# Optimization experiments

Hardware: AMD Instinct MI355X
Metric: run time of the kernel (lower is better)

## Reference

```python
import jax, jax.numpy as jnp
import numpy as np

ADAPT_RATE = 0.05


def setup_inputs() -> dict:
    key = jax.random.key(0)
    k1, k2, k3 = jax.random.split(key, 3)
    B, T, DIN, DOUT = 64, 256, 1024, 1024
    x = jax.random.normal(k1, (B, T, DIN), dtype=jnp.float32)
    W = jax.random.normal(k2, (DOUT, DIN), dtype=jnp.float32) / np.sqrt(DIN)
    b = jax.random.normal(k3, (DOUT,), dtype=jnp.float32) * 0.01
    threshold = jnp.ones((DOUT,), dtype=jnp.float32)
    return {"x": x, "W": W, "b": b, "threshold": threshold}


def reference(x, W, b, threshold):
    # Precompute the per-timestep linear once as a single big GEMM: [B,T,O]
    pre = jnp.einsum('bti,oi->bto', x, W) + b
    B, T, O = pre.shape

    def step(carry, pre_t):
        mem, thr = carry
        mem = mem + pre_t                       # membrane accumulate [B,O]
        s = (mem >= thr).astype(pre_t.dtype)    # hard threshold spike
        # adaptive threshold: in-place .data update in torch (no grad path)
        thr = thr + ADAPT_RATE * (s.mean(axis=0) - 0.5)
        mem = mem * (1.0 - s)                   # reset where spiked
        return (mem, thr), s

    mem0 = jnp.zeros((B, O), dtype=x.dtype)
    (_, _), spikes = jax.lax.scan(step, (mem0, threshold), jnp.swapaxes(pre, 0, 1))
    return jnp.swapaxes(spikes, 0, 1)  # [B,T,O]
```

## Files before the change

### kernel.cpp

```cpp
#include <hip/hip_runtime.h>

#define B_ 64
#define T_ 256
#define DIN_ 1024
#define DOUT_ 1024

typedef int v4i  __attribute__((ext_vector_type(4)));
typedef int v16i __attribute__((ext_vector_type(16)));

#define PRE_BYTES 134217728ULL
#define XS_BYTES  83886080ULL
#define WSL_BYTES 5242880ULL
#define SPM_BYTES 2097152ULL

__device__ __forceinline__ void async_copy16(const void* g, void* l) {
    __builtin_amdgcn_global_load_lds(
        (const __attribute__((address_space(1))) void*)g,
        (__attribute__((address_space(3))) void*)l, 16, 0, 0);
}

__global__ __launch_bounds__(256) void snn_split_x(
    const float* __restrict__ x, char* __restrict__ xs)
{
    const int W    = blockIdx.x * 4 + (threadIdx.x >> 6);
    const int lane = threadIdx.x & 63;
    const int mt = W & 1, kt = (W >> 1) & 31, t0 = W >> 6;
    const int m = lane & 31, kh = lane >> 5;
    const int b = mt * 32 + m;

    const float* src = x + ((size_t)b * T_ + t0) * DIN_ + kt * 32 + kh * 16;
    float f[16];
    *(float4*)(f)      = *(const float4*)(src);
    *(float4*)(f + 4)  = *(const float4*)(src + 4);
    *(float4*)(f + 8)  = *(const float4*)(src + 8);
    *(float4*)(f + 12) = *(const float4*)(src + 12);

    unsigned pk[5][4];
#pragma unroll
    for (int s = 0; s < 5; ++s)
        pk[s][0] = pk[s][1] = pk[s][2] = pk[s][3] = 0u;
#pragma unroll
    for (int j = 0; j < 16; ++j) {
        float v = f[j] * 0.125f;
#pragma unroll
        for (int s = 0; s < 5; ++s) {
            const float ml = (s == 0) ? 64.f : 128.f;
            const float sv = __builtin_rintf(v * ml);
            v = v * ml - sv;
            const int iv = (int)sv;
            pk[s][j >> 2] |= ((unsigned)iv & 0xffu) << ((j & 3) * 8);
        }
    }
#pragma unroll
    for (int s = 0; s < 5; ++s) {
        char* dst = xs + (size_t)(((s * 256 + t0) * 32 + kt) * 2 + mt) * 1024
                       + lane * 16;
        *(uint4*)dst = make_uint4(pk[s][0], pk[s][1], pk[s][2], pk[s][3]);
    }
}

__global__ __launch_bounds__(256) void snn_split_w(
    const float* __restrict__ Wt, char* __restrict__ wsl)
{
    const int W    = blockIdx.x * 4 + (threadIdx.x >> 6);
    const int lane = threadIdx.x & 63;
    const int kt = W & 31, ot = W >> 5;
    const int n = lane & 31, kh = lane >> 5;
    const int o = ot * 32 + n;

    const float* src = Wt + (size_t)o * DIN_ + kt * 32 + kh * 16;
    float f[16];
    *(float4*)(f)      = *(const float4*)(src);
    *(float4*)(f + 4)  = *(const float4*)(src + 4);
    *(float4*)(f + 8)  = *(const float4*)(src + 8);
    *(float4*)(f + 12) = *(const float4*)(src + 12);

    unsigned pk[5][4];
#pragma unroll
    for (int s = 0; s < 5; ++s)
        pk[s][0] = pk[s][1] = pk[s][2] = pk[s][3] = 0u;
#pragma unroll
    for (int j = 0; j < 16; ++j) {
        float v = f[j] * 4.0f;
#pragma unroll
        for (int s = 0; s < 5; ++s) {
            const float ml = (s == 0) ? 64.f : 128.f;
            const float sv = __builtin_rintf(v * ml);
            v = v * ml - sv;
            const int iv = (int)sv;
            pk[s][j >> 2] |= ((unsigned)iv & 0xffu) << ((j & 3) * 8);
        }
    }
#pragma unroll
    for (int s = 0; s < 5; ++s) {
        char* dst = wsl + (size_t)((s * 32 + ot) * 32 + kt) * 1024 + lane * 16;
        *(uint4*)dst = make_uint4(pk[s][0], pk[s][1], pk[s][2], pk[s][3]);
    }
}

__global__ __launch_bounds__(256, 3) void snn_gemm_i8(
    const char* __restrict__ xs, const char* __restrict__ wsl,
    const float* __restrict__ bias, double* __restrict__ pre)
{
    __shared__ __align__(16) char lds[2][20 * 1024];
    const int t0 = blockIdx.x >> 4;
    const int oB = blockIdx.x & 15;
    const int tid = threadIdx.x;
    const int lane = tid & 63;
    const int ws = __builtin_amdgcn_readfirstlane(tid >> 6);
    const int wmS = ws >> 1, woS = ws & 1;

    v16i zero;
#pragma unroll
    for (int r = 0; r < 16; ++r) zero[r] = 0;
    v16i acc[5];
#pragma unroll
    for (int g = 0; g < 5; ++g) acc[g] = zero;

    const char* gbase;
    size_t sStride;
    int ktStride, slot0;
    if (ws < 2) {
        gbase   = xs + ((size_t)t0 * 32 * 2 + ws) * 1024;
        sStride = 16777216;
        ktStride = 2048;
        slot0 = ws * 5;
    } else {
        gbase   = wsl + (size_t)(oB * 2 + (ws - 2)) * 32 * 1024;
        sStride = 1048576;
        ktStride = 1024;
        slot0 = 10 + (ws - 2) * 5;
    }
    const int lo = lane * 16;

#pragma unroll
    for (int s = 0; s < 5; ++s)
        async_copy16(gbase + (size_t)s * sStride + lo,
                     &lds[0][(slot0 + s) * 1024]);

    for (int kt = 0; kt < 32; ++kt) {
        __syncthreads();
        if (kt + 1 < 32) {
            const char* gn = gbase + (size_t)(kt + 1) * ktStride;
#pragma unroll
            for (int s = 0; s < 5; ++s)
                async_copy16(gn + (size_t)s * sStride + lo,
                             &lds[(kt + 1) & 1][(slot0 + s) * 1024]);
        }
        const char* abase = &lds[kt & 1][(wmS * 5) * 1024] + lo;
        const char* bbase = &lds[kt & 1][(10 + woS * 5) * 1024] + lo;
        v4i a[5], b[5];
#pragma unroll
        for (int s = 0; s < 5; ++s) {
            a[s] = *(const v4i*)(abase + s * 1024);
            b[s] = *(const v4i*)(bbase + s * 1024);
        }
#pragma unroll
        for (int i = 0; i < 5; ++i) {
#pragma unroll
            for (int j = 0; j < 5 - i; ++j)
                acc[i + j] = __builtin_amdgcn_mfma_i32_32x32x32_i8(
                    a[i], b[j], acc[i + j], 0, 0, 0);
        }
    }

    const int n = lane & 31, lh = lane >> 5;
    const int o = oB * 64 + woS * 32 + n;
    const double bv = (double)bias[o];
    double* dst = pre + ((size_t)t0 * DOUT_ + o) * 64 + wmS * 32;
#pragma unroll
    for (int r = 0; r < 16; ++r) {
        const int row = (r & 3) + 8 * (r >> 2) + 4 * lh;
        double v = (double)acc[4][r];
        v = v * 0.0078125 + (double)acc[3][r];
        v = v * 0.0078125 + (double)acc[2][r];
        v = v * 0.0078125 + (double)acc[1][r];
        v = v * 0.0078125 + (double)acc[0][r];
        dst[row] = v * 0x1p-11 + bv;
    }
}

__global__ __launch_bounds__(256, 2) void snn_gemm_fb(
    const float* __restrict__ x, const float* __restrict__ W,
    const float* __restrict__ bias, double* __restrict__ pre)
{
    __shared__ float smem[2][8 * 72 + 8 * 256];
    const int t0 = blockIdx.x & 255;
    const int o0 = blockIdx.x >> 8;
    const int tid = threadIdx.x;
    const int to = tid & 31;
    const int tb = tid >> 5;

    double acc[8][8];
#pragma unroll
    for (int i = 0; i < 8; ++i)
#pragma unroll
        for (int j = 0; j < 8; ++j) acc[i][j] = 0.0;

    const int arow = tid >> 2;
    const int ak2  = (tid & 3) * 2;
    const float* xg = x + (size_t)(t0 + 256 * arow) * DIN_ + ak2;
    const float* wg = W + (size_t)(o0 * 256 + tid) * DIN_;

    float2 f2  = *(const float2*)(xg);
    float4 bq0 = *(const float4*)(wg);
    float4 bq1 = *(const float4*)(wg + 4);

    for (int kc = 0; kc < DIN_ / 8; ++kc) {
        float* base = smem[kc & 1];
        float (*AsF)[72]  = (float(*)[72])base;
        float (*BsF)[256] = (float(*)[256])(base + 8 * 72);
        AsF[ak2 + 0][arow] = f2.x;
        AsF[ak2 + 1][arow] = f2.y;
        BsF[0][tid] = bq0.x;  BsF[1][tid] = bq0.y;
        BsF[2][tid] = bq0.z;  BsF[3][tid] = bq0.w;
        BsF[4][tid] = bq1.x;  BsF[5][tid] = bq1.y;
        BsF[6][tid] = bq1.z;  BsF[7][tid] = bq1.w;
        __syncthreads();
        if (kc + 1 < DIN_ / 8) {
            f2  = *(const float2*)(xg + (kc + 1) * 8);
            bq0 = *(const float4*)(wg + (kc + 1) * 8);
            bq1 = *(const float4*)(wg + (kc + 1) * 8 + 4);
        }
#pragma unroll
        for (int k = 0; k < 8; ++k) {
            const float4 af0 = *(const float4*)&AsF[k][tb * 8];
            const float4 af1 = *(const float4*)&AsF[k][tb * 8 + 4];
            const float4 bf0 = *(const float4*)&BsF[k][to * 4];
            const float4 bf1 = *(const float4*)&BsF[k][128 + to * 4];
            double a[8], b[8];
            a[0] = (double)af0.x; a[1] = (double)af0.y;
            a[2] = (double)af0.z; a[3] = (double)af0.w;
            a[4] = (double)af1.x; a[5] = (double)af1.y;
            a[6] = (double)af1.z; a[7] = (double)af1.w;
            b[0] = (double)bf0.x; b[1] = (double)bf0.y;
            b[2] = (double)bf0.z; b[3] = (double)bf0.w;
            b[4] = (double)bf1.x; b[5] = (double)bf1.y;
            b[6] = (double)bf1.z; b[7] = (double)bf1.w;
#pragma unroll
            for (int i = 0; i < 8; ++i)
#pragma unroll
                for (int j = 0; j < 8; ++j)
                    acc[i][j] += a[i] * b[j];
        }
    }

    double biasd[8];
#pragma unroll
    for (int j = 0; j < 8; ++j)
        biasd[j] = (double)bias[o0 * 256 + (j >> 2) * 128 + to * 4 + (j & 3)];
    double (*trans)[67] = (double(*)[67])smem[0];
    for (int c = 0; c < 16; ++c) {
        __syncthreads();
        const int j4  = c >> 3;
        const int tlo = (c & 7) * 4;
        if (to >= tlo && to < tlo + 4) {
#pragma unroll
            for (int p4 = 0; p4 < 4; ++p4) {
                const int r = (to - tlo) * 4 + p4;
                const int j = j4 * 4 + p4;
#pragma unroll
                for (int i = 0; i < 8; ++i)
                    trans[r][tb * 8 + i] = acc[i][j] + biasd[j];
            }
        }
        __syncthreads();
#pragma unroll
        for (int q = 0; q < 4; ++q) {
            const int idx = tid + 256 * q;
            const int b  = idx & 63;
            const int oc = idx >> 6;
            pre[(size_t)(t0 * DOUT_ + o0 * 256 + c * 16 + oc) * 64 + b] = trans[oc][b];
        }
    }
}

__global__ __launch_bounds__(256) void snn_scan(
    const double* __restrict__ pre, const float* __restrict__ thr_in,
    unsigned long long* __restrict__ spM, float* __restrict__ outD)
{
    const int wid  = (blockIdx.x * blockDim.x + threadIdx.x) >> 6;
    const int lane = threadIdx.x & 63;
    if (wid >= DOUT_) return;
    const int o = wid;

    double mem = 0.0;
    double thr = (double)thr_in[o];
    const double* p = pre + (size_t)o * 64 + lane;

    for (int t = 0; t < T_; t += 16) {
        double pv[16];
#pragma unroll
        for (int j = 0; j < 16; ++j)
            pv[j] = p[(size_t)(t + j) * (DOUT_ * 64)];
#pragma unroll
        for (int j = 0; j < 16; ++j) {
            mem += pv[j];
            const bool s = (mem >= thr);
            const unsigned long long msk = __ballot(s);
            const int cnt = __popcll(msk);
            thr += 0.05 * ((double)cnt * (1.0 / 64.0) - 0.5);
            if (spM) {
                if (lane == 0) spM[(size_t)(t + j) * DOUT_ + o] = msk;
            } else {
                outD[(size_t)lane * (T_ * DOUT_) + (size_t)(t + j) * DOUT_ + o] =
                    s ? 1.0f : 0.0f;
            }
            mem = s ? 0.0 : mem;
        }
    }
}

__global__ __launch_bounds__(256) void snn_expand(
    const unsigned long long* __restrict__ spM, float* __restrict__ out)
{
    const int r = blockIdx.x * 256 + threadIdx.x;
    const unsigned long long m = spM[r];
#pragma unroll
    for (int b = 0; b < 64; ++b)
        out[(size_t)b * (T_ * DOUT_) + r] = (float)((m >> b) & 1ULL);
}

extern "C" void kernel_launch(void* const* d_in, const int* in_sizes, int n_in,
                              void* d_out, int out_size, void* d_ws, size_t ws_size,
                              hipStream_t stream) {
    const float* x    = (const float*)d_in[0];
    const float* W    = (const float*)d_in[1];
    const float* bias = (const float*)d_in[2];
    const float* thr  = (const float*)d_in[3];
    float* out = (float*)d_out;

    double* pre = (double*)d_ws;
    const size_t need = PRE_BYTES + XS_BYTES + WSL_BYTES + SPM_BYTES;

    if (ws_size >= need) {
        char* xs  = (char*)d_ws + PRE_BYTES;
        char* wsl = xs + XS_BYTES;
        unsigned long long* spM = (unsigned long long*)(wsl + WSL_BYTES);
        snn_split_x<<<4096, 256, 0, stream>>>(x, xs);
        snn_split_w<<<256, 256, 0, stream>>>(W, wsl);
        snn_gemm_i8<<<4096, 256, 0, stream>>>(xs, wsl, bias, pre);
        snn_scan<<<256, 256, 0, stream>>>(pre, thr, spM, nullptr);
        snn_expand<<<1024, 256, 0, stream>>>(spM, out);
    } else {
        const bool two_stage = (ws_size >= PRE_BYTES + SPM_BYTES);
        unsigned long long* spM =
            two_stage ? (unsigned long long*)((char*)d_ws + PRE_BYTES) : nullptr;
        snn_gemm_fb<<<1024, 256, 0, stream>>>(x, W, bias, pre);
        snn_scan<<<256, 256, 0, stream>>>(pre, thr, spM, two_stage ? nullptr : out);
        if (two_stage)
            snn_expand<<<1024, 256, 0, stream>>>(spM, out);
    }
}
```

Before: 407.5 us.

## Widen int8 GEMM block tile to 128 outputs so each wave reuses A across two tiles

The split-int8 GEMM block tile grows from 64x64 to 64x128 outputs. Each wave now computes two 32x32 output tiles and reuses its A fragments across both, which halves the grid and the redundant loads of the x slices. The cost is more LDS per block (30KB double-buffered), twice the accumulator registers, and occupancy bounds lowered from 3 to 2 blocks per CU.

```diff
diff --git a/kernel.cpp b/kernel.cpp
--- a/kernel.cpp
+++ b/kernel.cpp
@@ -98,85 +98,104 @@
     }
 }
 
-__global__ __launch_bounds__(256, 3) void snn_gemm_i8(
+__global__ __launch_bounds__(256, 2) void snn_gemm_i8(
     const char* __restrict__ xs, const char* __restrict__ wsl,
     const float* __restrict__ bias, double* __restrict__ pre)
 {
-    __shared__ __align__(16) char lds[2][20 * 1024];
-    const int t0 = blockIdx.x >> 4;
-    const int oB = blockIdx.x & 15;
+    __shared__ __align__(16) char lds[2][30 * 1024];
+    const int t0 = blockIdx.x >> 3;
+    const int oB = blockIdx.x & 7;
     const int tid = threadIdx.x;
     const int lane = tid & 63;
     const int ws = __builtin_amdgcn_readfirstlane(tid >> 6);
-    const int wmS = ws >> 1, woS = ws & 1;
+    const int wm  = ws >> 1;
+    const int wop = (ws & 1) * 2;
 
     v16i zero;
 #pragma unroll
     for (int r = 0; r < 16; ++r) zero[r] = 0;
-    v16i acc[5];
-#pragma unroll
-    for (int g = 0; g < 5; ++g) acc[g] = zero;
-
-    const char* gbase;
-    size_t sStride;
-    int ktStride, slot0;
+    v16i acc[2][5];
+#pragma unroll
+    for (int p = 0; p < 2; ++p)
+#pragma unroll
+        for (int g = 0; g < 5; ++g) acc[p][g] = zero;
+
+    const int lo = lane * 16;
+
+    const char* agbase = xs + ((size_t)t0 * 32 * 2 + ws) * 1024;
+    const char* bgbase = wsl + (size_t)(oB * 4 + (ws - 2) * 2) * 32 * 1024;
+
     if (ws < 2) {
-        gbase   = xs + ((size_t)t0 * 32 * 2 + ws) * 1024;
-        sStride = 16777216;
-        ktStride = 2048;
-        slot0 = ws * 5;
+#pragma unroll
+        for (int s = 0; s < 5; ++s)
+            async_copy16(agbase + (size_t)s * 16777216 + lo,
+                         &lds[0][(ws * 5 + s) * 1024]);
     } else {
-        gbase   = wsl + (size_t)(oB * 2 + (ws - 2)) * 32 * 1024;
-        sStride = 1048576;
-        ktStride = 1024;
-        slot0 = 10 + (ws - 2) * 5;
-    }
-    const int lo = lane * 16;
-
-#pragma unroll
-    for (int s = 0; s < 5; ++s)
-        async_copy16(gbase + (size_t)s * sStride + lo,
-                     &lds[0][(slot0 + s) * 1024]);
+#pragma unroll
+        for (int o2 = 0; o2 < 2; ++o2)
+#pragma unroll
+            for (int s = 0; s < 5; ++s)
+                async_copy16(bgbase + (size_t)o2 * 32768 + (size_t)s * 1048576 + lo,
+                             &lds[0][(10 + ((ws - 2) * 2 + o2) * 5 + s) * 1024]);
+    }
 
     for (int kt = 0; kt < 32; ++kt) {
         __syncthreads();
         if (kt + 1 < 32) {
-            const char* gn = gbase + (size_t)(kt + 1) * ktStride;
+            char* buf = lds[(kt + 1) & 1];
+            if (ws < 2) {
+                const char* g = agbase + (size_t)(kt + 1) * 2048;
+#pragma unroll
+                for (int s = 0; s < 5; ++s)
+                    async_copy16(g + (size_t)s * 16777216 + lo,
+                                 &buf[(ws * 5 + s) * 1024]);
+            } else {
+                const char* g = bgbase + (size_t)(kt + 1) * 1024;
+#pragma unroll
+                for (int o2 = 0; o2 < 2; ++o2)
+#pragma unroll
+                    for (int s = 0; s < 5; ++s)
+                        async_copy16(g + (size_t)o2 * 32768 + (size_t)s * 1048576 + lo,
+                                     &buf[(10 + ((ws - 2) * 2 + o2) * 5 + s) * 1024]);
+            }
+        }
+        const char* cbuf = lds[kt & 1];
+        v4i a[5];
+#pragma unroll
+        for (int s = 0; s < 5; ++s)
+            a[s] = *(const v4i*)(cbuf + (wm * 5 + s) * 1024 + lo);
+#pragma unroll
+        for (int o2 = 0; o2 < 2; ++o2) {
+            v4i b[5];
 #pragma unroll
             for (int s = 0; s < 5; ++s)
-                async_copy16(gn + (size_t)s * sStride + lo,
-                             &lds[(kt + 1) & 1][(slot0 + s) * 1024]);
-        }
-        const char* abase = &lds[kt & 1][(wmS * 5) * 1024] + lo;
-        const char* bbase = &lds[kt & 1][(10 + woS * 5) * 1024] + lo;
-        v4i a[5], b[5];
-#pragma unroll
-        for (int s = 0; s < 5; ++s) {
-            a[s] = *(const v4i*)(abase + s * 1024);
-            b[s] = *(const v4i*)(bbase + s * 1024);
-        }
-#pragma unroll
-        for (int i = 0; i < 5; ++i) {
-#pragma unroll
-            for (int j = 0; j < 5 - i; ++j)
-                acc[i + j] = __builtin_amdgcn_mfma_i32_32x32x32_i8(
-                    a[i], b[j], acc[i + j], 0, 0, 0);
+                b[s] = *(const v4i*)(cbuf + (10 + (wop + o2) * 5 + s) * 1024 + lo);
+#pragma unroll
+            for (int i = 0; i < 5; ++i) {
+#pragma unroll
+                for (int j = 0; j < 5 - i; ++j)
+                    acc[o2][i + j] = __builtin_amdgcn_mfma_i32_32x32x32_i8(
+                        a[i], b[j], acc[o2][i + j], 0, 0, 0);
+            }
         }
     }
 
     const int n = lane & 31, lh = lane >> 5;
-    const int o = oB * 64 + woS * 32 + n;
-    const double bv = (double)bias[o];
-    double* dst = pre + ((size_t)t0 * DOUT_ + o) * 64 + wmS * 32;
-#pragma unroll
-    for (int r = 0; r < 16; ++r) {
-        const int row = (r & 3) + 8 * (r >> 2) + 4 * lh;
-        double v = (double)acc[4][r];
-        v = v * 0.0078125 + (double)acc[3][r];
-        v = v * 0.0078125 + (double)acc[2][r];
-        v = v * 0.0078125 + (double)acc[1][r];
-        v = v * 0.0078125 + (double)acc[0][r];
-        dst[row] = v * 0x1p-11 + bv;
+#pragma unroll
+    for (int o2 = 0; o2 < 2; ++o2) {
+        const int o = oB * 128 + (wop + o2) * 32 + n;
+        const double bv = (double)bias[o];
+        double* dst = pre + ((size_t)t0 * DOUT_ + o) * 64 + wm * 32;
+#pragma unroll
+        for (int r = 0; r < 16; ++r) {
+            const int row = (r & 3) + 8 * (r >> 2) + 4 * lh;
+            double v = (double)acc[o2][4][r];
+            v = v * 0.0078125 + (double)acc[o2][3][r];
+            v = v * 0.0078125 + (double)acc[o2][2][r];
+            v = v * 0.0078125 + (double)acc[o2][1][r];
+            v = v * 0.0078125 + (double)acc[o2][0][r];
+            dst[row] = v * 0x1p-11 + bv;
+        }
     }
 }
 
@@ -339,7 +358,7 @@
         unsigned long long* spM = (unsigned long long*)(wsl + WSL_BYTES);
         snn_split_x<<<4096, 256, 0, stream>>>(x, xs);
         snn_split_w<<<256, 256, 0, stream>>>(W, wsl);
-        snn_gemm_i8<<<4096, 256, 0, stream>>>(xs, wsl, bias, pre);
+        snn_gemm_i8<<<2048, 256, 0, stream>>>(xs, wsl, bias, pre);
         snn_scan<<<256, 256, 0, stream>>>(pre, thr, spM, nullptr);
         snn_expand<<<1024, 256, 0, stream>>>(spM, out);
     } else {
```

Measured after the change: 396.2 us. -2.8%, faster.

## Triple-buffer LDS in int8 GEMM with explicit vmcnt waits

Applied to the files above, without the earlier changes.

Replaces the double-buffered LDS loop in the int8 split-GEMM with a three-buffer rotation. Loads are issued two k-tiles ahead, and each stage waits with an explicit s_waitcnt vmcnt(5) plus a raw barrier, instead of a full __syncthreads that drains all outstanding loads. This keeps more global-to-LDS traffic in flight behind the MFMA work. In exchange LDS use rises from 40KB to 60KB per block and the occupancy hint drops from 3 to 2 blocks per CU.

```diff
diff --git a/kernel.cpp b/kernel.cpp
--- a/kernel.cpp
+++ b/kernel.cpp
@@ -98,17 +98,21 @@
     }
 }
 
-__global__ __launch_bounds__(256, 3) void snn_gemm_i8(
+__global__ __launch_bounds__(256, 2) void snn_gemm_i8(
     const char* __restrict__ xs, const char* __restrict__ wsl,
     const float* __restrict__ bias, double* __restrict__ pre)
 {
-    __shared__ __align__(16) char lds[2][20 * 1024];
+    __shared__ __align__(16) char ldsA[20 * 1024];
+    __shared__ __align__(16) char ldsB[20 * 1024];
+    __shared__ __align__(16) char ldsC[20 * 1024];
+
     const int t0 = blockIdx.x >> 4;
     const int oB = blockIdx.x & 15;
     const int tid = threadIdx.x;
     const int lane = tid & 63;
     const int ws = __builtin_amdgcn_readfirstlane(tid >> 6);
-    const int wmS = ws >> 1, woS = ws & 1;
+    const int wm5 = (ws >> 1) * 5;
+    const int wo5 = 10 + (ws & 1) * 5;
 
     v16i zero;
 #pragma unroll
@@ -117,57 +121,82 @@
 #pragma unroll
     for (int g = 0; g < 5; ++g) acc[g] = zero;
 
-    const char* gbase;
+    const char* gsrc;
     size_t sStride;
     int ktStride, slot0;
     if (ws < 2) {
-        gbase   = xs + ((size_t)t0 * 32 * 2 + ws) * 1024;
+        gsrc    = xs + ((size_t)t0 * 32 * 2 + ws) * 1024;
         sStride = 16777216;
         ktStride = 2048;
         slot0 = ws * 5;
     } else {
-        gbase   = wsl + (size_t)(oB * 2 + (ws - 2)) * 32 * 1024;
+        gsrc    = wsl + (size_t)(oB * 2 + (ws - 2)) * 32 * 1024;
         sStride = 1048576;
         ktStride = 1024;
         slot0 = 10 + (ws - 2) * 5;
     }
     const int lo = lane * 16;
 
-#pragma unroll
-    for (int s = 0; s < 5; ++s)
-        async_copy16(gbase + (size_t)s * sStride + lo,
-                     &lds[0][(slot0 + s) * 1024]);
-
-    for (int kt = 0; kt < 32; ++kt) {
-        __syncthreads();
-        if (kt + 1 < 32) {
-            const char* gn = gbase + (size_t)(kt + 1) * ktStride;
-#pragma unroll
-            for (int s = 0; s < 5; ++s)
-                async_copy16(gn + (size_t)s * sStride + lo,
-                             &lds[(kt + 1) & 1][(slot0 + s) * 1024]);
-        }
-        const char* abase = &lds[kt & 1][(wmS * 5) * 1024] + lo;
-        const char* bbase = &lds[kt & 1][(10 + woS * 5) * 1024] + lo;
-        v4i a[5], b[5];
-#pragma unroll
-        for (int s = 0; s < 5; ++s) {
-            a[s] = *(const v4i*)(abase + s * 1024);
-            b[s] = *(const v4i*)(bbase + s * 1024);
-        }
-#pragma unroll
-        for (int i = 0; i < 5; ++i) {
-#pragma unroll
-            for (int j = 0; j < 5 - i; ++j)
-                acc[i + j] = __builtin_amdgcn_mfma_i32_32x32x32_i8(
-                    a[i], b[j], acc[i + j], 0, 0, 0);
-        }
-    }
+#define DMA_KT(BUF, ktv)                                                     \
+    {                                                                        \
+        const char* g_ = gsrc + (size_t)(ktv) * ktStride;                    \
+        _Pragma("unroll")                                                    \
+        for (int s_ = 0; s_ < 5; ++s_)                                       \
+            async_copy16(g_ + (size_t)s_ * sStride + lo,                     \
+                         &BUF[(slot0 + s_) * 1024]);                         \
+    }
+
+#define COMPUTE_KT(BUF)                                                      \
+    {                                                                        \
+        v4i a_[5], b_[5];                                                    \
+        _Pragma("unroll")                                                    \
+        for (int s_ = 0; s_ < 5; ++s_) {                                     \
+            a_[s_] = *(const v4i*)(&BUF[(wm5 + s_) * 1024] + lo);            \
+            b_[s_] = *(const v4i*)(&BUF[(wo5 + s_) * 1024] + lo);            \
+        }                                                                    \
+        _Pragma("unroll")                                                    \
+        for (int i_ = 0; i_ < 5; ++i_) {                                     \
+            _Pragma("unroll")                                                \
+            for (int j_ = 0; j_ < 5 - i_; ++j_)                              \
+                acc[i_ + j_] = __builtin_amdgcn_mfma_i32_32x32x32_i8(        \
+                    a_[i_], b_[j_], acc[i_ + j_], 0, 0, 0);                  \
+        }                                                                    \
+    }
+
+#define STAGE(RBUF, WBUF, ktv)                                               \
+    {                                                                        \
+        asm volatile("s_waitcnt vmcnt(5)" ::: "memory");                     \
+        __builtin_amdgcn_s_barrier();                                        \
+        DMA_KT(WBUF, (ktv) + 2);                                             \
+        COMPUTE_KT(RBUF);                                                    \
+    }
+
+    DMA_KT(ldsA, 0);
+    DMA_KT(ldsB, 1);
+
+    for (int kt = 0; kt < 28; kt += 3) {
+        STAGE(ldsA, ldsC, kt);
+        STAGE(ldsB, ldsA, kt + 1);
+        STAGE(ldsC, ldsB, kt + 2);
+    }
+    {
+        asm volatile("s_waitcnt vmcnt(5)" ::: "memory");
+        __builtin_amdgcn_s_barrier();
+        COMPUTE_KT(ldsA);
+    }
+    {
+        asm volatile("s_waitcnt vmcnt(0)" ::: "memory");
+        __builtin_amdgcn_s_barrier();
+        COMPUTE_KT(ldsB);
+    }
+#undef STAGE
+#undef COMPUTE_KT
+#undef DMA_KT
 
     const int n = lane & 31, lh = lane >> 5;
-    const int o = oB * 64 + woS * 32 + n;
+    const int o = oB * 64 + (ws & 1) * 32 + n;
     const double bv = (double)bias[o];
-    double* dst = pre + ((size_t)t0 * DOUT_ + o) * 64 + wmS * 32;
+    double* dst = pre + ((size_t)t0 * DOUT_ + o) * 64 + (ws >> 1) * 32;
 #pragma unroll
     for (int r = 0; r < 16; ++r) {
         const int row = (r & 3) + 8 * (r >> 2) + 4 * lh;
```

After: 397.2 us. 1.03x faster.
